# Performance work log

Hardware: AMD Instinct MI355X
Metric: run time of the kernel (lower is better)

## Reference

```python
import jax, jax.numpy as jnp
import numpy as np

N, D1, D2, B = 8, 2048, 1024, 512
D = D1 * D2
MAXBW = 3
NUM_PART = 5          # num_possible_partitions
TEMP = 0.01           # TEMPERATURE used in df_lt
DENOS = (3.0, 5.0, 17.0)  # 2^2-1, 2^2+1, 2^4+1


def ste_floor(x):
    # straight-through floor: forward floor, backward identity
    return x + jax.lax.stop_gradient(jnp.floor(x) - x)


def segmented_mean(piece, scheme, msp):
    """Replicates the inner python scan over sorted rows.
    piece:  (N, D) sorted residual errors
    scheme: (N-1, D) rounded split decisions (0/1), per column
    msp:    (N-1, D) soft split probabilities (grad factors), per column
    Returns (N, D): each row gets grad_ * (segment mean) of its segment.
    """
    n = piece.shape[0]
    buf = jnp.zeros_like(piece[0])
    cnt = jnp.zeros_like(piece[0])
    g = jnp.ones_like(piece[0])
    reset = jnp.zeros(piece.shape[1], dtype=bool)
    vlist, blist = [], []
    for i in range(n):
        buf = jnp.where(reset, piece[i], buf + piece[i])
        cnt = jnp.where(reset, 1.0, cnt + 1.0)
        g = jnp.where(reset, 1.0, g)
        if i == n - 1:
            vlist.append(g * (buf / cnt))
            blist.append(jnp.ones_like(reset))
        else:
            b = scheme[i] > 0.5
            vlist.append(jnp.where(b, g * msp[i], 0.0) * (buf / cnt))
            blist.append(b)
            g = jnp.where(b, g, g * (1.0 - msp[i]))
            reset = b
    # broadcast each segment-end value back to all rows of its segment
    out = vlist[-1]
    outs = [out]
    for i in range(n - 2, -1, -1):
        out = jnp.where(blist[i], vlist[i], out)
        outs.append(out)
    return jnp.stack(outs[::-1], axis=0)


def residual_quant(U, vsum, s, thr):
    """One residual quantization level (the update_partition=True branch)."""
    res = U - vsum                                   # (N, D)
    idx_maps = jnp.argsort(res, axis=0)              # torch.sort ascending, dim=0
    sorted_err = jnp.take_along_axis(res, idx_maps, axis=0)
    delta = sorted_err[1:] - sorted_err[:-1]         # (N-1, D), >= 0
    delta = delta / jnp.max(delta)
    msp = jax.nn.sigmoid((delta - thr) / TEMP)       # mean_split_point (N-1, D)
    rs = jnp.round(msp)                              # round_split, 0/1

    nm1 = N - 1
    P = 2 ** nm1  # all possible split-column patterns (torch.unique over dim=1)
    weights = (2 ** jnp.arange(nm1 - 1, -1, -1)).astype(jnp.int32)  # row 0 = MSB (lexicographic)
    code = jnp.sum(rs.astype(jnp.int32) * weights[:, None], axis=0)  # (D,)
    counts = jnp.zeros((P,), jnp.int32).at[code].add(1)
    present = counts > 0
    # torch.unique sorts patterns lexicographically -> rank = #present codes below
    rank_of_code = jnp.cumsum(present.astype(jnp.int32)) - present.astype(jnp.int32)
    order = jnp.argsort(-counts)                     # codes by count descending
    top_codes = order[:NUM_PART]
    top_ranks = rank_of_code[top_codes]              # s_indices[:NUM_PART]
    # binary patterns for every possible code
    patterns = ((jnp.arange(P)[:, None] >> jnp.arange(nm1 - 1, -1, -1)[None, :]) & 1).astype(jnp.float32)  # (P, N-1)
    inter = patterns @ patterns[top_codes].T         # (P, NUM_PART)
    sel = jnp.argmax(inter, axis=1)
    reassigned = top_ranks[sel]                      # (P,)
    is_top = jnp.any(rank_of_code[:, None] == top_ranks[None, :], axis=1)
    final_rank = jnp.where(is_top, rank_of_code, reassigned)  # (P,)
    c_rank = final_rank[code]                        # clustered_indices, (D,)

    # NOTE: original indexes round_split / mean_split_point columns BY the
    # unique-cluster index value s_idx (a quirk of the source); replicate it.
    scheme_used = rs[:, c_rank]                      # (N-1, D)
    msp_used = msp[:, c_rank]                        # (N-1, D)

    inner = segmented_mean(sorted_err, scheme_used, msp_used)  # (N, D)
    # einsum('cb,cba->ab', inner, one_hot(idx_maps)) == unsort along dim 0
    inv = jnp.argsort(idx_maps, axis=0)
    grouped = jnp.take_along_axis(inner, inv, axis=0)
    return s * ste_floor(grouped / s)


def setup_inputs():
    key = jax.random.key(0)
    k1, k2 = jax.random.split(key)
    x = jax.random.normal(k1, (B, N, D1), dtype=jnp.float32)
    # kaiming_normal_ on (N, D): std = sqrt(2 / fan_in), fan_in = D
    U = jax.random.normal(k2, (N, D), dtype=jnp.float32) * np.float32(np.sqrt(2.0 / D))
    thres_mean = jnp.full((D2,), -1.3, dtype=jnp.float32)
    return {"x": x, "U": U, "thres_mean": thres_mean}


def reference(x, U, thres_mean):
    beta = jnp.max(U)
    alpha = jnp.min(U)
    s = (beta - alpha) / DENOS[0]
    vsum = s * ste_floor(U / s)                      # base quantization level
    thr = jax.nn.sigmoid(jnp.repeat(thres_mean, D1))  # thres_mean.repeat_interleave(D1)
    for deno in DENOS[1:MAXBW]:
        s = s / deno
        vsum = vsum + residual_quant(U, vsum, s, thr)
    w = vsum.reshape(N, D1, D2)
    return jnp.einsum('bnd,ndl->bnl', x, w)
```

## Files before the change

### kernel.cpp

```cpp
#include <hip/hip_runtime.h>
#include <hip/hip_bf16.h>
#include <math.h>

#define NROW 8
#define DT   2097152
#define DD1  2048
#define DD2  1024
#define BATCH 512
#define NBLK 2048


typedef __attribute__((ext_vector_type(8))) short short8;
typedef __attribute__((ext_vector_type(4))) float f32x4;

__device__ __forceinline__ unsigned fenc(float f){
  unsigned u = __float_as_uint(f);
  return (u & 0x80000000u) ? ~u : (u | 0x80000000u);
}
__device__ __forceinline__ float fdec(unsigned k){
  return (k & 0x80000000u) ? __uint_as_float(k ^ 0x80000000u) : __uint_as_float(~k);
}
__device__ __forceinline__ float sigmoid_ref(float z){
  #pragma clang fp contract(off)
  return 1.0f / (1.0f + expf(-z));
}
__device__ __forceinline__ unsigned short f2bf(float f){
  __hip_bfloat16 h = __float2bfloat16(f);
  return *reinterpret_cast<unsigned short*>(&h);
}
__device__ __forceinline__ float base1(float u, float s1, float inv_s1){
  #pragma clang fp contract(off)
  return s1 * floorf(u * inv_s1);
}
__device__ __forceinline__ float vn2_of(float u, unsigned char mb, float s1, float inv_s1, float s2){
  #pragma clang fp contract(off)
  return base1(u, s1, inv_s1) + s2 * (float)((int)mb - 8);
}
__device__ __forceinline__ void async16(const unsigned short* g, unsigned short* l){
  __builtin_amdgcn_global_load_lds((const __attribute__((address_space(1))) unsigned int*)g,
                                   (__attribute__((address_space(3))) unsigned int*)l, 16, 0, 0);
}

#define CSWAPV(a,b) { float _lo=fminf(a,b), _hi=fmaxf(a,b); a=_lo; b=_hi; }
__device__ __forceinline__ void sort8v(float v[8]){
  CSWAPV(v[0],v[1]) CSWAPV(v[2],v[3]) CSWAPV(v[4],v[5]) CSWAPV(v[6],v[7])
  CSWAPV(v[0],v[2]) CSWAPV(v[1],v[3]) CSWAPV(v[4],v[6]) CSWAPV(v[5],v[7])
  CSWAPV(v[1],v[2]) CSWAPV(v[5],v[6])
  CSWAPV(v[0],v[4]) CSWAPV(v[1],v[5]) CSWAPV(v[2],v[6]) CSWAPV(v[3],v[7])
  CSWAPV(v[2],v[4]) CSWAPV(v[3],v[5])
  CSWAPV(v[1],v[2]) CSWAPV(v[3],v[4]) CSWAPV(v[5],v[6])
}
__device__ __forceinline__ void cswapkv(float&av,int&ai,float&bv,int&bi){
  bool sw = (av > bv) || ((av == bv) && (ai > bi));
  float nav = sw ? bv : av; float nbv = sw ? av : bv;
  int   nai = sw ? bi : ai; int   nbi = sw ? ai : bi;
  av = nav; bv = nbv; ai = nai; bi = nbi;
}
#define CSWAPK(i,j) cswapkv(v[i],ix[i],v[j],ix[j]);
__device__ __forceinline__ void sort8kv(float v[8], int ix[8]){
  CSWAPK(0,1) CSWAPK(2,3) CSWAPK(4,5) CSWAPK(6,7)
  CSWAPK(0,2) CSWAPK(1,3) CSWAPK(4,6) CSWAPK(5,7)
  CSWAPK(1,2) CSWAPK(5,6)
  CSWAPK(0,4) CSWAPK(1,5) CSWAPK(2,6) CSWAPK(3,7)
  CSWAPK(2,4) CSWAPK(3,5)
  CSWAPK(1,2) CSWAPK(3,4) CSWAPK(5,6)
}

__global__ __launch_bounds__(256) void k_mmxb(const float* __restrict__ U, const float* __restrict__ x,
                                              unsigned short* __restrict__ xb,
                                              unsigned* __restrict__ meta, unsigned* __restrict__ fin){
  __shared__ unsigned redA[256], redB[256];
  int t = threadIdx.x, b = blockIdx.x;
  int gid = b*256 + t;
  if (b == 0 && t < 128){ meta[4+t] = 0u; meta[132+t] = 0u; }
  const float4* x4 = (const float4*)x;
  #pragma unroll
  for (int i = 0; i < 4; ++i){
    int idx = gid + i*524288;
    float4 v = x4[idx];
    ushort4 o;
    o.x = f2bf(v.x); o.y = f2bf(v.y); o.z = f2bf(v.z); o.w = f2bf(v.w);
    *(ushort4*)(xb + (size_t)idx*4) = o;
  }
  const float4* U4 = (const float4*)U;
  float mx = -INFINITY, mn = INFINITY;
  #pragma unroll
  for (int i = 0; i < 8; ++i){
    float4 v = U4[gid + i*524288];
    mx = fmaxf(mx, fmaxf(fmaxf(v.x,v.y), fmaxf(v.z,v.w)));
    mn = fminf(mn, fminf(fminf(v.x,v.y), fminf(v.z,v.w)));
  }
  redA[t] = fenc(mx); redB[t] = fenc(mn);
  __syncthreads();
  for (int o = 128; o > 0; o >>= 1){
    if (t < o){ redA[t] = max(redA[t], redA[t+o]); redB[t] = min(redB[t], redB[t+o]); }
    __syncthreads();
  }
  if (t == 0){ atomicMax(&fin[0], redA[0]); atomicMin(&fin[3], redB[0]); }
}

__global__ __launch_bounds__(256) void k_passA2(const float* __restrict__ U,
                                                unsigned* __restrict__ fin){
  #pragma clang fp contract(off)
  __shared__ unsigned red[256];
  int t = threadIdx.x, b = blockIdx.x;
  float s1 = (fdec(fin[0]) - fdec(fin[3])) / 3.0f;
  float inv_s1 = 1.0f / s1;
  int d0 = (b*256 + t)*4;
  float4 u[8];
  #pragma unroll
  for (int i = 0; i < 8; ++i) u[i] = *(const float4*)(U + (size_t)i*DT + d0);
  unsigned dmax = 0u;
  #pragma unroll
  for (int c = 0; c < 4; ++c){
    float res[8];
    #pragma unroll
    for (int i = 0; i < 8; ++i){
      float uv = ((const float*)&u[i])[c];
      res[i] = uv - base1(uv, s1, inv_s1);
    }
    sort8v(res);
    float m = 0.0f;
    #pragma unroll
    for (int i = 0; i < 7; ++i) m = fmaxf(m, res[i+1] - res[i]);
    dmax = max(dmax, __float_as_uint(m));
  }
  red[t] = dmax;
  __syncthreads();
  for (int o = 128; o > 0; o >>= 1){
    if (t < o) red[t] = max(red[t], red[t+o]);
    __syncthreads();
  }
  if (t == 0) atomicMax(&fin[1], red[0]);
}

template<int LEVEL>
__global__ __launch_bounds__(256) void k_passB(const float* __restrict__ U,
                                               const unsigned char* __restrict__ mcode,
                                               const float* __restrict__ tm,
                                               unsigned char* __restrict__ code,
                                               unsigned* __restrict__ meta,
                                               const unsigned* __restrict__ fin){
  #pragma clang fp contract(off)
  __shared__ int hist[128];
  int t = threadIdx.x, b = blockIdx.x;
  int lane = t & 63;
  if (t < 128) hist[t] = 0;
  float s1 = (fdec(fin[0]) - fdec(fin[3])) / 3.0f;
  float inv_s1 = 1.0f / s1;
  float s2 = s1 / 5.0f;
  float gmax = __uint_as_float(fin[(LEVEL==2)?1:2]);
  float inv_gmax = 1.0f / gmax;
  int d0 = (b*256 + t)*4;
  float4 u[8], bb[8];
  #pragma unroll
  for (int i = 0; i < 8; ++i){
    u[i] = *(const float4*)(U + (size_t)i*DT + d0);
    if (LEVEL == 2){
      bb[i].x = base1(u[i].x, s1, inv_s1); bb[i].y = base1(u[i].y, s1, inv_s1);
      bb[i].z = base1(u[i].z, s1, inv_s1); bb[i].w = base1(u[i].w, s1, inv_s1);
    } else {
      uchar4 m4 = *(const uchar4*)(mcode + (size_t)i*DT + d0);
      bb[i].x = vn2_of(u[i].x, m4.x, s1, inv_s1, s2);
      bb[i].y = vn2_of(u[i].y, m4.y, s1, inv_s1, s2);
      bb[i].z = vn2_of(u[i].z, m4.z, s1, inv_s1, s2);
      bb[i].w = vn2_of(u[i].w, m4.w, s1, inv_s1, s2);
    }
  }
  __syncthreads();
  float thr = sigmoid_ref(tm[d0 >> 11]);
  uchar4 cods;
  unsigned char* cp = (unsigned char*)&cods;
  #pragma unroll
  for (int c = 0; c < 4; ++c){
    float res[8];
    #pragma unroll
    for (int i = 0; i < 8; ++i) res[i] = ((const float*)&u[i])[c] - ((const float*)&bb[i])[c];
    sort8v(res);
    int cd = 0;
    #pragma unroll
    for (int i = 0; i < 7; ++i){
      float dn = (res[i+1] - res[i]) * inv_gmax;
      cd = (cd << 1) | ((dn > thr) ? 1 : 0);
    }
    cp[c] = (unsigned char)cd;
    unsigned long long mset = ~0ull;
    #pragma unroll
    for (int bi = 0; bi < 7; ++bi){
      bool bit = ((cd >> bi) & 1) != 0;
      unsigned long long bbm = __ballot(bit);
      mset &= bit ? bbm : ~bbm;
    }
    int leader = (int)__ffsll(mset) - 1;
    if (lane == leader) atomicAdd(&hist[cd], (int)__popcll(mset));
  }
  *(uchar4*)(code + d0) = cods;
  __syncthreads();
  if (t < 128){ int h = hist[t]; if (h) atomicAdd((int*)&meta[((LEVEL==2)?4:132) + t], h); }
}

template<int LEVEL>
__global__ void k_small(const float* __restrict__ U, const unsigned char* __restrict__ mcode,
                        const float* __restrict__ tm, unsigned* __restrict__ meta,
                        const unsigned* __restrict__ fin){
  #pragma clang fp contract(off)
  __shared__ int cs[128], rk[128], redk[128];
  __shared__ int top_code[5], top_rank[5];
  __shared__ int w0cnt;
  int c = threadIdx.x;
  float s1 = (fdec(fin[0]) - fdec(fin[3])) / 3.0f;
  float inv_s1 = 1.0f / s1;
  float s2 = s1 / 5.0f;
  float gmax = __uint_as_float(fin[(LEVEL==2)?1:2]);
  cs[c] = (int)meta[((LEVEL==2)?4:132) + c];
  bool present = cs[c] > 0;
  unsigned long long bm = __ballot(present);
  int lane = c & 63;
  int r = (int)__popcll(bm & ((1ull << lane) - 1ull));
  if (c == 63) w0cnt = (int)__popcll(bm);
  __syncthreads();
  if (c >= 64) r += w0cnt;
  rk[c] = r;
  __syncthreads();
  for (int k = 0; k < 5; ++k){
    redk[c] = (cs[c] << 7) | (127 - c);
    __syncthreads();
    for (int o = 64; o > 0; o >>= 1){
      if (c < o) redk[c] = max(redk[c], redk[c+o]);
      __syncthreads();
    }
    if (c == 0){
      int best = 127 - (redk[0] & 127);
      top_code[k] = best; top_rank[k] = rk[best];
      cs[best] = -1;
    }
    __syncthreads();
  }
  int besti = -1, sel = 0;
  #pragma unroll
  for (int j = 0; j < 5; ++j){
    int inter = __popc(c & top_code[j]);
    if (inter > besti){ besti = inter; sel = j; }
  }
  bool is_top = false;
  #pragma unroll
  for (int j = 0; j < 5; ++j) is_top = is_top || (rk[c] == top_rank[j]);
  ((int*)meta)[260 + c] = is_top ? rk[c] : top_rank[sel];
  float res[8];
  #pragma unroll
  for (int i = 0; i < 8; ++i){
    size_t off = (size_t)i*DT + c;
    float u = U[off];
    float bval = (LEVEL==2) ? base1(u, s1, inv_s1) : vn2_of(u, mcode[off], s1, inv_s1, s2);
    res[i] = u - bval;
  }
  sort8v(res);
  float thr = sigmoid_ref(tm[c >> 11]);
  unsigned bits = 0;
  float* msp_tab = (float*)(meta + 388);
  #pragma unroll
  for (int i = 0; i < 7; ++i){
    float dn  = (res[i+1] - res[i]) / gmax;
    float z   = (dn - thr) / 0.01f;
    float msp = sigmoid_ref(z);
    msp_tab[c*7 + i] = msp;
    bits |= ((unsigned)(int)rintf(msp)) << i;
  }
  meta[1284 + c] = bits;
}

template<int LEVEL>
__global__ __launch_bounds__(256) void k_passD(const float* __restrict__ U,
                                               unsigned char* __restrict__ mcode,
                                               unsigned short* __restrict__ vsumb,
                                               const unsigned char* __restrict__ code,
                                               unsigned* __restrict__ meta,
                                               unsigned* __restrict__ fin){
  #pragma clang fp contract(off)
  __shared__ float qcol[8*256];
  __shared__ unsigned red[256];
  __shared__ int fr_s[128];
  __shared__ unsigned bits_s[128];
  __shared__ float msp_s[896];
  int t = threadIdx.x, b = blockIdx.x;
  float s1 = (fdec(fin[0]) - fdec(fin[3])) / 3.0f;
  float inv_s1 = 1.0f / s1;
  float s2 = s1 / 5.0f;
  float s  = (LEVEL == 2) ? s2 : (s2 / 17.0f);
  float inv_s = 1.0f / s;
  if (t < 128){ fr_s[t] = ((const int*)meta)[260+t]; bits_s[t] = meta[1284+t]; }
  for (int i = t; i < 896; i += 256) msp_s[i] = ((const float*)(meta+388))[i];
  __syncthreads();
  int d0 = (b*256 + t)*4;
  float4 u4[8];
  uchar4 m4[8];
  #pragma unroll
  for (int i = 0; i < 8; ++i){
    u4[i] = *(const float4*)(U + (size_t)i*DT + d0);
    if (LEVEL == 3) m4[i] = *(const uchar4*)(mcode + (size_t)i*DT + d0);
  }
  uchar4 cods = *(const uchar4*)(code + d0);
  const unsigned char* cp = (const unsigned char*)&cods;
  uchar4 mout[8];
  ushort4 ov[8];
  unsigned dmax = 0u;
  #pragma unroll
  for (int c = 0; c < 4; ++c){
    float v[8]; int ix[8];
    #pragma unroll
    for (int i = 0; i < 8; ++i){
      float uv = ((const float*)&u4[i])[c];
      float bval;
      if (LEVEL == 2) bval = base1(uv, s1, inv_s1);
      else {
        int mi = (int)((const unsigned char*)&m4[i])[c] - 8;
        bval = base1(uv, s1, inv_s1) + s2 * (float)mi;
      }
      v[i] = uv - bval;
      ix[i] = i;
    }
    sort8kv(v, ix);
    int cr = fr_s[cp[c]];
    unsigned sb = bits_s[cr];
    float vv[8]; bool bl[8];
    float buf = 0.0f, cnt = 0.0f, g = 1.0f; bool reset = false;
    #pragma unroll
    for (int i = 0; i < 8; ++i){
      buf = reset ? v[i] : (buf + v[i]);
      cnt = reset ? 1.0f : (cnt + 1.0f);
      g   = reset ? 1.0f : g;
      float m = buf * __builtin_amdgcn_rcpf(cnt);
      if (i == 7){ vv[7] = g * m; bl[7] = true; }
      else {
        float msp = msp_s[cr*7 + i];
        bool bv = ((sb >> i) & 1u) != 0u;
        vv[i] = bv ? ((g * msp) * m) : 0.0f;
        bl[i] = bv;
        g = bv ? g : (g * (1.0f - msp));
        reset = bv;
      }
    }
    float out = vv[7];
    float inner[8];
    inner[7] = out;
    for (int i = 6; i >= 0; --i){ if (bl[i]) out = vv[i]; inner[i] = out; }
    if (LEVEL == 2){
      unsigned mp = 0u;
      #pragma unroll
      for (int i = 0; i < 8; ++i){
        float mf = floorf(inner[i] * inv_s);
        int mi = (int)mf;
        mi = max(-8, min(7, mi));
        mp |= (unsigned)(mi + 8) << (4*ix[i]);
      }
      float res3[8];
      #pragma unroll
      for (int r = 0; r < 8; ++r){
        int mi = (int)((mp >> (4*r)) & 15u) - 8;
        ((unsigned char*)&mout[r])[c] = (unsigned char)(mi + 8);
        float uv = ((const float*)&u4[r])[c];
        float qv = s * (float)mi;
        float vn = base1(uv, s1, inv_s1) + qv;
        res3[r] = uv - vn;
      }
      sort8v(res3);
      float m = 0.0f;
      #pragma unroll
      for (int i = 0; i < 7; ++i) m = fmaxf(m, res3[i+1] - res3[i]);
      dmax = max(dmax, __float_as_uint(m));
    } else {
      #pragma unroll
      for (int i = 0; i < 8; ++i) qcol[ix[i]*256 + t] = floorf(inner[i] * inv_s);
      #pragma unroll
      for (int r = 0; r < 8; ++r){
        int mi = (int)((const unsigned char*)&m4[r])[c] - 8;
        float uv = ((const float*)&u4[r])[c];
        float bv = base1(uv, s1, inv_s1) + s2 * (float)mi;
        float qv = s * qcol[r*256 + t];
        ((unsigned short*)&ov[r])[c] = f2bf(bv + qv);
      }
    }
  }
  if (LEVEL == 2){
    #pragma unroll
    for (int r = 0; r < 8; ++r)
      *(uchar4*)(mcode + (size_t)r*DT + d0) = mout[r];
    red[t] = dmax;
    __syncthreads();
    for (int o = 128; o > 0; o >>= 1){
      if (t < o) red[t] = max(red[t], red[t+o]);
      __syncthreads();
    }
    if (t == 0) atomicMax(&fin[2], red[0]);
  } else {
    #pragma unroll
    for (int r = 0; r < 8; ++r)
      *(ushort4*)(vsumb + (size_t)r*DT + d0) = ov[r];
  }
}

__global__ __launch_bounds__(256) void k_wt(const unsigned short* __restrict__ vsumb,
                                            unsigned short* __restrict__ wt){
  __shared__ unsigned short tile[64][68];
  int t = threadIdx.x;
  int c4 = t & 15, r0 = t >> 4;
  int n = blockIdx.z, k0 = blockIdx.y*64, l0 = blockIdx.x*64;
  const unsigned short* src = vsumb + (size_t)n*DT;
  #pragma unroll
  for (int i = 0; i < 4; ++i){
    int r = r0 + i*16;
    ushort4 v = *(const ushort4*)(src + (size_t)(k0+r)*DD2 + l0 + c4*4);
    *(ushort4*)&tile[r][c4*4] = v;
  }
  __syncthreads();
  unsigned short* dst = wt + (size_t)n*DT;
  #pragma unroll
  for (int i = 0; i < 4; ++i){
    int rl = r0 + i*16;
    ushort4 o;
    o.x = tile[c4*4+0][rl]; o.y = tile[c4*4+1][rl];
    o.z = tile[c4*4+2][rl]; o.w = tile[c4*4+3][rl];
    *(ushort4*)(dst + (size_t)(l0+rl)*DD1 + k0 + c4*4) = o;
  }
}

__global__ __launch_bounds__(256) void k_gemm(const unsigned short* __restrict__ xb,
                                              const unsigned short* __restrict__ wt,
                                              float* __restrict__ out){
  __shared__ __align__(16) unsigned short As[64*64];
  __shared__ __align__(16) unsigned short Bs[128*64];
  int t = threadIdx.x;
  int lane = t & 63, wv = t >> 6;
  int n  = blockIdx.z;
  int b0 = blockIdx.y * 64;
  int l0 = blockIdx.x * 128;
  int wm = (wv >> 1) * 32, wn = (wv & 1) * 64;
  int col = lane & 15, quad = lane >> 4;
  int arow = lane >> 3, aseg = lane & 7;
  const unsigned short* wtn = wt + (size_t)n*DT;
  f32x4 acc[2][4] = {};
  for (int k0 = 0; k0 < DD1; k0 += 64){
    #pragma unroll
    for (int i = 0; i < 2; ++i){
      int row = wv*16 + i*8 + arow;
      const unsigned short* g = xb + (((size_t)(b0+row)*NROW + n)*DD1 + k0 + aseg*8);
      async16(g, &As[(wv*16 + i*8)*64]);
    }
    #pragma unroll
    for (int i = 0; i < 4; ++i){
      int row = wv*32 + i*8 + arow;
      const unsigned short* g = wtn + ((size_t)(l0+row)*DD1 + k0 + aseg*8);
      async16(g, &Bs[(wv*32 + i*8)*64]);
    }
    __syncthreads();
    #pragma unroll
    for (int ks = 0; ks < 2; ++ks){
      int kq = ks*32 + quad*8;
      short8 af[2], bfr[4];
      #pragma unroll
      for (int mi = 0; mi < 2; ++mi) af[mi]  = *(const short8*)&As[(wm + mi*16 + col)*64 + kq];
      #pragma unroll
      for (int ni = 0; ni < 4; ++ni) bfr[ni] = *(const short8*)&Bs[(wn + ni*16 + col)*64 + kq];
      #pragma unroll
      for (int mi = 0; mi < 2; ++mi)
        #pragma unroll
        for (int ni = 0; ni < 4; ++ni)
          acc[mi][ni] = __builtin_amdgcn_mfma_f32_16x16x32_bf16(af[mi], bfr[ni], acc[mi][ni], 0, 0, 0);
    }
    __syncthreads();
  }
  #pragma unroll
  for (int mi = 0; mi < 2; ++mi)
    #pragma unroll
    for (int ni = 0; ni < 4; ++ni)
      #pragma unroll
      for (int r = 0; r < 4; ++r){
        int bb = b0 + wm + mi*16 + quad*4 + r;
        int l = l0 + wn + ni*16 + col;
        out[((size_t)bb*NROW + n)*DD2 + l] = acc[mi][ni][r];
      }
}

extern "C" void kernel_launch(void* const* d_in, const int* in_sizes, int n_in,
                              void* d_out, int out_size, void* d_ws, size_t ws_size,
                              hipStream_t stream){
  const float* x  = (const float*)d_in[0];
  const float* U  = (const float*)d_in[1];
  const float* tm = (const float*)d_in[2];
  float* out = (float*)d_out;
  unsigned char*  mcode = (unsigned char*)d_ws;
  unsigned short* vsumb = (unsigned short*)((unsigned char*)d_ws + 16777216);
  unsigned short* xb    = (unsigned short*)((unsigned char*)d_ws + 50331648);
  unsigned char*  code  = (unsigned char*)d_ws + 67108864;
  unsigned short* wt    = (unsigned short*)((unsigned char*)d_ws + 69206016);
  unsigned* meta  = (unsigned*)((unsigned char*)d_ws + 102760448);
  unsigned* fin   = (unsigned*)((unsigned char*)d_ws + 102801408);
  (void)in_sizes; (void)n_in; (void)out_size; (void)ws_size;

  hipMemsetAsync(fin, 0, 12, stream);
  hipMemsetAsync(fin + 3, 0xFF, 4, stream);
  k_mmxb    <<<NBLK, 256, 0, stream>>>(U, x, xb, meta, fin);
  k_passA2  <<<NBLK, 256, 0, stream>>>(U, fin);
  k_passB<2><<<NBLK, 256, 0, stream>>>(U, mcode, tm, code, meta, fin);
  k_small<2><<<1,   128, 0, stream>>>(U, mcode, tm, meta, fin);
  k_passD<2><<<NBLK, 256, 0, stream>>>(U, mcode, vsumb, code, meta, fin);
  k_passB<3><<<NBLK, 256, 0, stream>>>(U, mcode, tm, code, meta, fin);
  k_small<3><<<1,   128, 0, stream>>>(U, mcode, tm, meta, fin);
  k_passD<3><<<NBLK, 256, 0, stream>>>(U, mcode, vsumb, code, meta, fin);
  k_wt  <<<dim3(DD2/64, DD1/64, NROW), 256, 0, stream>>>(vsumb, wt);
  k_gemm<<<dim3(DD2/128, BATCH/64, NROW), 256, 0, stream>>>(xb, wt, out);
}
```

Measured before the change: 401.3 us.

## Fold single-block partition selection into passD and merge memsets

```diff
diff --git a/kernel.cpp b/kernel.cpp
--- a/kernel.cpp
+++ b/kernel.cpp
@@ -19,6 +19,10 @@
 }
 __device__ __forceinline__ float fdec(unsigned k){
   return (k & 0x80000000u) ? __uint_as_float(k ^ 0x80000000u) : __uint_as_float(~k);
+}
+__device__ __forceinline__ float s1_of(const unsigned* fin){
+  #pragma clang fp contract(off)
+  return (fdec(fin[0]) - fdec(~fin[3])) / 3.0f;
 }
 __device__ __forceinline__ float sigmoid_ref(float z){
   #pragma clang fp contract(off)
@@ -74,21 +78,23 @@
   int gid = b*256 + t;
   if (b == 0 && t < 128){ meta[4+t] = 0u; meta[132+t] = 0u; }
   const float4* x4 = (const float4*)x;
+  const float4* U4 = (const float4*)U;
+  float4 xv[4], uv[8];
+  #pragma unroll
+  for (int i = 0; i < 4; ++i) xv[i] = x4[gid + i*524288];
+  #pragma unroll
+  for (int i = 0; i < 8; ++i) uv[i] = U4[gid + i*524288];
   #pragma unroll
   for (int i = 0; i < 4; ++i){
-    int idx = gid + i*524288;
-    float4 v = x4[idx];
     ushort4 o;
-    o.x = f2bf(v.x); o.y = f2bf(v.y); o.z = f2bf(v.z); o.w = f2bf(v.w);
-    *(ushort4*)(xb + (size_t)idx*4) = o;
-  }
-  const float4* U4 = (const float4*)U;
+    o.x = f2bf(xv[i].x); o.y = f2bf(xv[i].y); o.z = f2bf(xv[i].z); o.w = f2bf(xv[i].w);
+    *(ushort4*)(xb + (size_t)(gid + i*524288)*4) = o;
+  }
   float mx = -INFINITY, mn = INFINITY;
   #pragma unroll
   for (int i = 0; i < 8; ++i){
-    float4 v = U4[gid + i*524288];
-    mx = fmaxf(mx, fmaxf(fmaxf(v.x,v.y), fmaxf(v.z,v.w)));
-    mn = fminf(mn, fminf(fminf(v.x,v.y), fminf(v.z,v.w)));
+    mx = fmaxf(mx, fmaxf(fmaxf(uv[i].x,uv[i].y), fmaxf(uv[i].z,uv[i].w)));
+    mn = fminf(mn, fminf(fminf(uv[i].x,uv[i].y), fminf(uv[i].z,uv[i].w)));
   }
   redA[t] = fenc(mx); redB[t] = fenc(mn);
   __syncthreads();
@@ -96,7 +102,7 @@
     if (t < o){ redA[t] = max(redA[t], redA[t+o]); redB[t] = min(redB[t], redB[t+o]); }
     __syncthreads();
   }
-  if (t == 0){ atomicMax(&fin[0], redA[0]); atomicMin(&fin[3], redB[0]); }
+  if (t == 0){ atomicMax(&fin[0], redA[0]); atomicMax(&fin[3], ~redB[0]); }
 }
 
 __global__ __launch_bounds__(256) void k_passA2(const float* __restrict__ U,
@@ -104,7 +110,7 @@
   #pragma clang fp contract(off)
   __shared__ unsigned red[256];
   int t = threadIdx.x, b = blockIdx.x;
-  float s1 = (fdec(fin[0]) - fdec(fin[3])) / 3.0f;
+  float s1 = s1_of(fin);
   float inv_s1 = 1.0f / s1;
   int d0 = (b*256 + t)*4;
   float4 u[8];
@@ -146,7 +152,7 @@
   int t = threadIdx.x, b = blockIdx.x;
   int lane = t & 63;
   if (t < 128) hist[t] = 0;
-  float s1 = (fdec(fin[0]) - fdec(fin[3])) / 3.0f;
+  float s1 = s1_of(fin);
   float inv_s1 = 1.0f / s1;
   float s2 = s1 / 5.0f;
   float gmax = __uint_as_float(fin[(LEVEL==2)?1:2]);
@@ -200,80 +206,11 @@
 }
 
 template<int LEVEL>
-__global__ void k_small(const float* __restrict__ U, const unsigned char* __restrict__ mcode,
-                        const float* __restrict__ tm, unsigned* __restrict__ meta,
-                        const unsigned* __restrict__ fin){
-  #pragma clang fp contract(off)
-  __shared__ int cs[128], rk[128], redk[128];
-  __shared__ int top_code[5], top_rank[5];
-  __shared__ int w0cnt;
-  int c = threadIdx.x;
-  float s1 = (fdec(fin[0]) - fdec(fin[3])) / 3.0f;
-  float inv_s1 = 1.0f / s1;
-  float s2 = s1 / 5.0f;
-  float gmax = __uint_as_float(fin[(LEVEL==2)?1:2]);
-  cs[c] = (int)meta[((LEVEL==2)?4:132) + c];
-  bool present = cs[c] > 0;
-  unsigned long long bm = __ballot(present);
-  int lane = c & 63;
-  int r = (int)__popcll(bm & ((1ull << lane) - 1ull));
-  if (c == 63) w0cnt = (int)__popcll(bm);
-  __syncthreads();
-  if (c >= 64) r += w0cnt;
-  rk[c] = r;
-  __syncthreads();
-  for (int k = 0; k < 5; ++k){
-    redk[c] = (cs[c] << 7) | (127 - c);
-    __syncthreads();
-    for (int o = 64; o > 0; o >>= 1){
-      if (c < o) redk[c] = max(redk[c], redk[c+o]);
-      __syncthreads();
-    }
-    if (c == 0){
-      int best = 127 - (redk[0] & 127);
-      top_code[k] = best; top_rank[k] = rk[best];
-      cs[best] = -1;
-    }
-    __syncthreads();
-  }
-  int besti = -1, sel = 0;
-  #pragma unroll
-  for (int j = 0; j < 5; ++j){
-    int inter = __popc(c & top_code[j]);
-    if (inter > besti){ besti = inter; sel = j; }
-  }
-  bool is_top = false;
-  #pragma unroll
-  for (int j = 0; j < 5; ++j) is_top = is_top || (rk[c] == top_rank[j]);
-  ((int*)meta)[260 + c] = is_top ? rk[c] : top_rank[sel];
-  float res[8];
-  #pragma unroll
-  for (int i = 0; i < 8; ++i){
-    size_t off = (size_t)i*DT + c;
-    float u = U[off];
-    float bval = (LEVEL==2) ? base1(u, s1, inv_s1) : vn2_of(u, mcode[off], s1, inv_s1, s2);
-    res[i] = u - bval;
-  }
-  sort8v(res);
-  float thr = sigmoid_ref(tm[c >> 11]);
-  unsigned bits = 0;
-  float* msp_tab = (float*)(meta + 388);
-  #pragma unroll
-  for (int i = 0; i < 7; ++i){
-    float dn  = (res[i+1] - res[i]) / gmax;
-    float z   = (dn - thr) / 0.01f;
-    float msp = sigmoid_ref(z);
-    msp_tab[c*7 + i] = msp;
-    bits |= ((unsigned)(int)rintf(msp)) << i;
-  }
-  meta[1284 + c] = bits;
-}
-
-template<int LEVEL>
 __global__ __launch_bounds__(256) void k_passD(const float* __restrict__ U,
                                                unsigned char* __restrict__ mcode,
                                                unsigned short* __restrict__ vsumb,
                                                const unsigned char* __restrict__ code,
+                                               const float* __restrict__ tm,
                                                unsigned* __restrict__ meta,
                                                unsigned* __restrict__ fin){
   #pragma clang fp contract(off)
@@ -282,15 +219,80 @@
   __shared__ int fr_s[128];
   __shared__ unsigned bits_s[128];
   __shared__ float msp_s[896];
+  __shared__ int cs[128], rk[128], redk[128];
+  __shared__ int top_code[5], top_rank[5];
+  __shared__ int w0cnt;
   int t = threadIdx.x, b = blockIdx.x;
-  float s1 = (fdec(fin[0]) - fdec(fin[3])) / 3.0f;
+  float s1 = s1_of(fin);
   float inv_s1 = 1.0f / s1;
   float s2 = s1 / 5.0f;
   float s  = (LEVEL == 2) ? s2 : (s2 / 17.0f);
   float inv_s = 1.0f / s;
-  if (t < 128){ fr_s[t] = ((const int*)meta)[260+t]; bits_s[t] = meta[1284+t]; }
-  for (int i = t; i < 896; i += 256) msp_s[i] = ((const float*)(meta+388))[i];
+  float gmax = __uint_as_float(fin[(LEVEL==2)?1:2]);
+
+  {
+    int c = t;
+    int lane = t & 63;
+    if (c < 128){
+      cs[c] = (int)meta[((LEVEL==2)?4:132) + c];
+      bool present = cs[c] > 0;
+      unsigned long long bm = __ballot(present);
+      int r = (int)__popcll(bm & ((1ull << lane) - 1ull));
+      if (c == 63) w0cnt = (int)__popcll(bm);
+      rk[c] = r;
+    }
+    __syncthreads();
+    if (c >= 64 && c < 128) rk[c] += w0cnt;
+    __syncthreads();
+    for (int k = 0; k < 5; ++k){
+      if (c < 128) redk[c] = (cs[c] << 7) | (127 - c);
+      __syncthreads();
+      for (int o = 64; o > 0; o >>= 1){
+        if (c < o) redk[c] = max(redk[c], redk[c+o]);
+        __syncthreads();
+      }
+      if (c == 0){
+        int best = 127 - (redk[0] & 127);
+        top_code[k] = best; top_rank[k] = rk[best];
+        cs[best] = -1;
+      }
+      __syncthreads();
+    }
+    if (c < 128){
+      int besti = -1, sel = 0;
+      #pragma unroll
+      for (int j = 0; j < 5; ++j){
+        int inter = __popc(c & top_code[j]);
+        if (inter > besti){ besti = inter; sel = j; }
+      }
+      bool is_top = false;
+      #pragma unroll
+      for (int j = 0; j < 5; ++j) is_top = is_top || (rk[c] == top_rank[j]);
+      fr_s[c] = is_top ? rk[c] : top_rank[sel];
+      float res[8];
+      #pragma unroll
+      for (int i = 0; i < 8; ++i){
+        size_t off = (size_t)i*DT + c;
+        float uu = U[off];
+        float bval = (LEVEL==2) ? base1(uu, s1, inv_s1) : vn2_of(uu, mcode[off], s1, inv_s1, s2);
+        res[i] = uu - bval;
+      }
+      sort8v(res);
+      float thr = sigmoid_ref(tm[c >> 11]);
+      unsigned bits = 0;
+      #pragma unroll
+      for (int i = 0; i < 7; ++i){
+        float dn  = (res[i+1] - res[i]) / gmax;
+        float z   = (dn - thr) / 0.01f;
+        float msp = sigmoid_ref(z);
+        msp_s[c*7 + i] = msp;
+        bits |= ((unsigned)(int)rintf(msp)) << i;
+      }
+      bits_s[c] = bits;
+    }
+  }
   __syncthreads();
+
   int d0 = (b*256 + t)*4;
   float4 u4[8];
   uchar4 m4[8];
@@ -497,16 +499,13 @@
   unsigned* fin   = (unsigned*)((unsigned char*)d_ws + 102801408);
   (void)in_sizes; (void)n_in; (void)out_size; (void)ws_size;
 
-  hipMemsetAsync(fin, 0, 12, stream);
-  hipMemsetAsync(fin + 3, 0xFF, 4, stream);
+  hipMemsetAsync(fin, 0, 16, stream);
   k_mmxb    <<<NBLK, 256, 0, stream>>>(U, x, xb, meta, fin);
   k_passA2  <<<NBLK, 256, 0, stream>>>(U, fin);
   k_passB<2><<<NBLK, 256, 0, stream>>>(U, mcode, tm, code, meta, fin);
-  k_small<2><<<1,   128, 0, stream>>>(U, mcode, tm, meta, fin);
-  k_passD<2><<<NBLK, 256, 0, stream>>>(U, mcode, vsumb, code, meta, fin);
+  k_passD<2><<<NBLK, 256, 0, stream>>>(U, mcode, vsumb, code, tm, meta, fin);
   k_passB<3><<<NBLK, 256, 0, stream>>>(U, mcode, tm, code, meta, fin);
-  k_small<3><<<1,   128, 0, stream>>>(U, mcode, tm, meta, fin);
-  k_passD<3><<<NBLK, 256, 0, stream>>>(U, mcode, vsumb, code, meta, fin);
+  k_passD<3><<<NBLK, 256, 0, stream>>>(U, mcode, vsumb, code, tm, meta, fin);
   k_wt  <<<dim3(DD2/64, DD1/64, NROW), 256, 0, stream>>>(vsumb, wt);
   k_gemm<<<dim3(DD2/128, BATCH/64, NROW), 256, 0, stream>>>(xb, wt, out);
 }
```

Measured after the change: 404.8 us. No clear change (+0.9%).
